# Optimization experiments

Hardware: AMD Instinct MI355X
Metric: run time of the kernel (lower is better)

The kernel has to match this reference:

```python
import jax, jax.numpy as jnp
import numpy as np

B = 8192; L = 68; NPG = L + 1; N = B * NPG
IN = 4; HID = 64; OUT = 7; NL = 8
BN_EPS = 1e-5


def setup_inputs() -> dict:
    key = jax.random.key(0)
    ks = jax.random.split(key, 12)
    # graph topology (same for every graph): ring among L landmarks + master node (idx L)
    # connected to every landmark; directed edges both ways (PyG-style edge_index).
    ring = np.stack([np.arange(L), (np.arange(L) + 1) % L])            # [2, L]
    mast = np.stack([np.arange(L), np.full(L, L)])                     # [2, L]
    und = np.concatenate([ring, mast], axis=1)                         # [2, 2L]
    e = np.concatenate([und, und[::-1]], axis=1)                       # [2, 4L]
    offs = (np.arange(B) * NPG)[:, None, None]
    edge_index = (e[None] + offs).transpose(1, 0, 2).reshape(2, -1)    # [2, B*4L]
    s = 1.0 / np.sqrt(HID)
    return {
        "x": jax.random.normal(ks[0], (N, IN), jnp.float32),
        "edge_index": jnp.asarray(edge_index, jnp.int32),
        "batch": jnp.repeat(jnp.arange(B, dtype=jnp.int32), NPG),
        "master_mask": jnp.tile(jnp.arange(NPG) == L, B),
        "conv_first_W": jax.random.normal(ks[1], (IN, HID), jnp.float32) * 0.5,
        "conv_first_b": jnp.zeros((HID,), jnp.float32),
        "conv_mid_W": jax.random.normal(ks[2], (NL - 2, HID, HID), jnp.float32) * s,
        "conv_mid_b": jnp.zeros((NL - 2, HID), jnp.float32),
        "conv_last_W": jax.random.normal(ks[3], (HID, HID), jnp.float32) * s,
        "conv_last_b": jnp.zeros((HID,), jnp.float32),
        "bn_gamma": jnp.ones((NL - 1, HID), jnp.float32),
        "bn_beta": jnp.zeros((NL - 1, HID), jnp.float32),
        "bn_mean": jax.random.normal(ks[4], (NL - 1, HID), jnp.float32) * 0.1,
        "bn_var": jax.random.uniform(ks[5], (NL - 1, HID), jnp.float32) * 0.5 + 0.5,
        "att_W1": jax.random.normal(ks[6], (HID, HID), jnp.float32) * s,
        "att_b1": jnp.zeros((HID,), jnp.float32),
        "att_W2": jax.random.normal(ks[7], (HID, 1), jnp.float32) * s,
        "att_b2": jnp.zeros((1,), jnp.float32),
        "fc1_W": jax.random.normal(ks[8], (3 * HID, HID), jnp.float32) / np.sqrt(3 * HID),
        "fc1_b": jnp.zeros((HID,), jnp.float32),
        "fc2_W": jax.random.normal(ks[9], (HID, OUT), jnp.float32) * s,
        "fc2_b": jnp.zeros((OUT,), jnp.float32),
    }


def reference(x, edge_index, batch, master_mask,
              conv_first_W, conv_first_b, conv_mid_W, conv_mid_b,
              conv_last_W, conv_last_b, bn_gamma, bn_beta, bn_mean, bn_var,
              att_W1, att_b1, att_W2, att_b2, fc1_W, fc1_b, fc2_W, fc2_b):
    n = x.shape[0]
    src, dst = edge_index[0], edge_index[1]
    # GCN symmetric normalization with self-loops: deg_i = 1 + in-degree
    deg = 1.0 + jax.ops.segment_sum(jnp.ones_like(src, x.dtype), dst, num_segments=n)
    dis = jax.lax.rsqrt(deg)
    enorm = (dis[src] * dis[dst])[:, None]                 # [E,1]
    self_norm = (1.0 / deg)[:, None]                       # [N,1] self-loop coeff

    def gcn(h, W, b):
        h = h @ W                                          # [N,HID]
        agg = jax.ops.segment_sum(h[src] * enorm, dst, num_segments=n)
        return agg + h * self_norm + b

    def bn(h, i):  # eval-mode BatchNorm1d
        return bn_gamma[i] * (h - bn_mean[i]) * jax.lax.rsqrt(bn_var[i] + BN_EPS) + bn_beta[i]

    h = bn(jax.nn.relu(gcn(x, conv_first_W, conv_first_b)), 0)
    for i in range(NL - 2):  # residual GCN blocks
        h = bn(jax.nn.relu(gcn(h, conv_mid_W[i], conv_mid_b[i])), i + 1) + h
    h = jax.nn.relu(gcn(h, conv_last_W, conv_last_b))

    mfl = master_mask.astype(h.dtype)                      # [N]
    mcnt = jax.ops.segment_sum(mfl, batch, num_segments=B)
    master = jax.ops.segment_sum(h * mfl[:, None], batch, num_segments=B) / mcnt[:, None]
    att = jax.nn.sigmoid(jax.nn.relu(master @ att_W1 + att_b1) @ att_W2 + att_b2)
    master = master * att

    rfl = 1.0 - mfl
    rcnt = jax.ops.segment_sum(rfl, batch, num_segments=B)
    x_mean = jax.ops.segment_sum(h * rfl[:, None], batch, num_segments=B) / rcnt[:, None]
    h_masked = jnp.where(master_mask[:, None], -jnp.inf, h)
    x_max = jax.ops.segment_max(h_masked, batch, num_segments=B)

    g = jnp.concatenate([x_mean, x_max, master], axis=1)   # [B, 3*HID]
    return jax.nn.relu(g @ fc1_W + fc1_b) @ fc2_W + fc2_b  # [B, OUT]
```

## Files before the change

kernel.cpp:

```cpp
#include <hip/hip_runtime.h>

typedef float f32x4 __attribute__((ext_vector_type(4)));
typedef short short8 __attribute__((ext_vector_type(8)));
typedef unsigned int u32;
typedef unsigned short u16;

#define CLL 0.25f
#define CML 0.06019292654288460f
#define SELFM 0.014492753623188406f

__device__ __forceinline__ u16 f2bf(float x) {
  u32 b = __float_as_uint(x);
  return (u16)((b + 0x7FFFu + ((b >> 16) & 1u)) >> 16);
}

__device__ __forceinline__ u32 cvtpk(float a, float b) {
  u32 r;
  asm("v_cvt_pk_bf16_f32 %0, %1, %2" : "=v"(r) : "v"(a), "v"(b));
  return r;
}

__global__ void prep(const float* __restrict__ midW, const float* __restrict__ lastW,
                     const float* __restrict__ bng, const float* __restrict__ bnb,
                     const float* __restrict__ bnm, const float* __restrict__ bnv,
                     u16* __restrict__ frag, float* __restrict__ bns) {
  const int t0 = blockIdx.x * blockDim.x + threadIdx.x;
  for (int u = t0; u < 7 * 4 * 2 * 64; u += gridDim.x * blockDim.x) {
    const int lane = u & 63;
    const int t = u >> 6;
    const int ks = t & 1;
    const int nt = (t >> 1) & 3;
    const int l = t >> 3;
    const float* W = (l < 6) ? (midW + l * 4096) : lastW;
    const int col = nt * 16 + (lane & 15);
    const int kb = ks * 32 + (lane >> 4) * 8;
    u16* dst = frag + (size_t)u * 8;
#pragma unroll
    for (int j = 0; j < 8; ++j) dst[j] = f2bf(W[(kb + j) * 64 + col]);
  }
  for (int u = t0; u < 7 * 64; u += gridDim.x * blockDim.x) {
    const int l = u >> 6, f = u & 63;
    const float sc = (float)((double)bng[l * 64 + f] / sqrt((double)bnv[l * 64 + f] + 1e-5));
    bns[l * 128 + f] = sc;
    bns[l * 128 + 64 + f] = bnb[l * 64 + f] - bnm[l * 64 + f] * sc;
  }
}

#define SUM4(V) ((V)[0] + (V)[1] + (V)[2] + (V)[3])
#define MAX4(V) fmaxf(fmaxf((V)[0], (V)[1]), fmaxf((V)[2], (V)[3]))

#define WADDR(MT, R) ((16 * (MT) + 4 * qg + (R)) * 64 + (cq ^ ((R) << 3)))

#define STEP(MT, T, TPM1, TNP1, H, RESID)                              \
  {                                                                    \
    const float sp = (qg == 3) ? TPM1[3] : T[3];                       \
    const float pv = __shfl(sp, (lane + 48) & 63, 64);                 \
    const float sn = (qg == 0) ? TNP1[0] : T[0];                       \
    const float nv = __shfl(sn, (lane + 16) & 63, 64);                 \
    const float ta0 = ((MT) == 0 && qg == 0) ? t4[3] : pv;             \
    const float tb3 = ((MT) == 4 && qg == 0) ? t0[0] : nv;             \
    float o0 = fmaf(CLL, ta0 + T[0] + T[1], cmt);                      \
    float o1 = fmaf(CLL, T[0] + T[1] + T[2], cmt);                     \
    float o2 = fmaf(CLL, T[1] + T[2] + T[3], cmt);                     \
    float o3 = fmaf(CLL, T[2] + T[3] + tb3, cmt);                      \
    o0 = fmaf(fmaxf(o0, 0.f), sc, sh);                                 \
    o1 = fmaf(fmaxf(o1, 0.f), sc, sh);                                 \
    o2 = fmaf(fmaxf(o2, 0.f), sc, sh);                                 \
    o3 = fmaf(fmaxf(o3, 0.f), sc, sh);                                 \
    if (RESID) { o0 += H[0]; o1 += H[1]; o2 += H[2]; o3 += H[3]; }     \
    H[0] = o0; H[1] = o1; H[2] = o2; H[3] = o3;                        \
  }

#define WPAIR(HW, MT, H)                                               \
  {                                                                    \
    const u32 pa = cvtpk(H[0], H[1]);                                  \
    const u32 pb = cvtpk(H[2], H[3]);                                  \
    (HW)[WADDR(MT, 0)] = (u16)pa;                                      \
    (HW)[WADDR(MT, 1)] = (u16)(pa >> 16);                              \
    (HW)[WADDR(MT, 2)] = (u16)pb;                                      \
    (HW)[WADDR(MT, 3)] = (u16)(pb >> 16);                              \
  }

#define EPILOG(RESID, WRITE, HBW)                                      \
  {                                                                    \
    float S = SUM4(t0) + SUM4(t1) + SUM4(t2) + SUM4(t3) + SUM4(t4);    \
    if (qg == 1) S -= t4[0];     \
    S += __shfl_xor(S, 16, 64);                                        \
    S += __shfl_xor(S, 32, 64);                                        \
    const float t68b = __shfl(t4[0], 16 + p15, 64);                    \
    const float cmt = fmaf(CML, t68b, bias);                           \
    float mv = fmaxf(fmaf(CML, S, fmaf(SELFM, t68b, bias)), 0.f);      \
    mv = fmaf(mv, sc, sh);                                             \
    if (RESID) mv += h4[0];                                            \
    STEP(0, t0, t4, t1, h0, RESID)                                     \
    STEP(1, t1, t0, t2, h1, RESID)                                     \
    STEP(2, t2, t1, t3, h2, RESID)                                     \
    STEP(3, t3, t2, t4, h3, RESID)                                     \
    STEP(4, t4, t3, t0, h4, RESID)                                     \
    if (qg == 1) h4[0] = mv;        \
    if (WRITE) {                                                       \
      u16* hw_ = (HBW);                                                \
      WPAIR(hw_, 0, h0)                                                \
      WPAIR(hw_, 1, h1)                                                \
      WPAIR(hw_, 2, h2)                                                \
      WPAIR(hw_, 3, h3)                                                \
      if (qg == 0) { WPAIR(hw_, 4, h4) }                               \
      else if (qg == 1) hw_[68 * 64 + (c ^ 32)] = (u16)cvtpk(h4[0], h4[0]); \
    }                                                                  \
  }

#define MP(HR, MT, T)                                                  \
  {                                                                    \
    const short8 a0 = *(const short8*)&(HR)[(MT) * 1024 + ra0];        \
    const short8 a1 = *(const short8*)&(HR)[(MT) * 1024 + ra1];        \
    f32x4 acc = {0.f, 0.f, 0.f, 0.f};                                  \
    acc = __builtin_amdgcn_mfma_f32_16x16x32_bf16(a0, b0, acc, 0, 0, 0); \
    acc = __builtin_amdgcn_mfma_f32_16x16x32_bf16(a1, b1, acc, 0, 0, 0); \
    T = acc;                                                           \
  }

__launch_bounds__(256)
__global__ void gcn_fused(
    const float* __restrict__ x,
    const float* __restrict__ cfW, const float* __restrict__ cfb,
    const float* __restrict__ cmb, const float* __restrict__ clb,
    const float* __restrict__ aW1, const float* __restrict__ ab1,
    const float* __restrict__ aW2, const float* __restrict__ ab2,
    const float* __restrict__ f1W, const float* __restrict__ f1b,
    const float* __restrict__ f2W, const float* __restrict__ f2b,
    const u16* __restrict__ frag, const float* __restrict__ bns,
    float* __restrict__ out) {
  __shared__ u16 hb[2][80 * 64];
  __shared__ float xl4[80 * 4];
  __shared__ float mrow[64];
  __shared__ float gv[192];
  __shared__ float part[256];

  const int tid = threadIdx.x;
  const int g = blockIdx.x;
  const int lane = tid & 63;
  const int wv = tid >> 6;
  const int p15 = lane & 15;
  const int qg = lane >> 4;
  const int c = wv * 16 + p15;
  const int cq = c ^ ((qg & 1) << 5);
  const int rsw = (p15 & 7) << 3;
  const int ra0 = (p15 * 64 + qg * 8) ^ rsw;
  const int ra1 = (p15 * 64 + 32 + qg * 8) ^ rsw;

  for (int i = tid; i < 5120; i += 256) ((u32*)hb)[i] = 0u;
  if (tid < 69)
    *(f32x4*)&xl4[tid * 4] = *(const f32x4*)&x[((size_t)g * 69 + tid) * 4];
  else if (tid < 80)
    *(f32x4*)&xl4[tid * 4] = (f32x4){0.f, 0.f, 0.f, 0.f};

  const u16* fb = frag + ((size_t)(0 * 4 + wv) * 2 * 64 + lane) * 8;
  short8 b0 = *(const short8*)fb;
  short8 b1 = *(const short8*)(fb + 512);

  f32x4 t0, t1, t2, t3, t4;
  f32x4 h0, h1, h2, h3, h4;

  __syncthreads();

  {
    const float w0 = cfW[c], w1 = cfW[64 + c], w2 = cfW[128 + c], w3 = cfW[192 + c];
#define L0T(MT, T)                                                     \
    { _Pragma("unroll") for (int r = 0; r < 4; ++r) {                  \
        const f32x4 xv = *(const f32x4*)&xl4[(16 * (MT) + 4 * qg + r) * 4]; \
        T[r] = fmaf(xv[0], w0, fmaf(xv[1], w1, fmaf(xv[2], w2, xv[3] * w3))); } }
    L0T(0, t0) L0T(1, t1) L0T(2, t2) L0T(3, t3) L0T(4, t4)
#undef L0T
  }
  {
    const float bias = cfb[c];
    const float sc = bns[c], sh = bns[64 + c];
    EPILOG(false, true, &hb[0][0])
  }
  __syncthreads();

  for (int l = 1; l <= 6; ++l) {
    const u16* fbn = frag + ((size_t)(l * 4 + wv) * 2 * 64 + lane) * 8;
    const short8 nb0 = *(const short8*)fbn;
    const short8 nb1 = *(const short8*)(fbn + 512);
    const u16* hr = &hb[(l + 1) & 1][0];
    MP(hr, 0, t0) MP(hr, 1, t1) MP(hr, 2, t2) MP(hr, 3, t3) MP(hr, 4, t4)
    b0 = nb0;
    b1 = nb1;
    const float bias = cmb[(l - 1) * 64 + c];
    const float sc = bns[l * 128 + c], sh = bns[l * 128 + 64 + c];
    EPILOG(true, true, &hb[l & 1][0])
    __syncthreads();
  }

  {
    const u16* hr = &hb[0][0];
    MP(hr, 0, t0) MP(hr, 1, t1) MP(hr, 2, t2) MP(hr, 3, t3) MP(hr, 4, t4)
    const float bias = clb[c];
    const float sc = 1.f, sh = 0.f;
    EPILOG(false, false, (u16*)nullptr)
  }

  {
    float s = SUM4(h0) + SUM4(h1) + SUM4(h2) + SUM4(h3);
    float mx = fmaxf(fmaxf(MAX4(h0), MAX4(h1)), fmaxf(MAX4(h2), MAX4(h3)));
    if (qg == 0) {
      s += SUM4(h4);
      mx = fmaxf(mx, MAX4(h4));
    }
    s += __shfl_xor(s, 16, 64);
    s += __shfl_xor(s, 32, 64);
    mx = fmaxf(mx, __shfl_xor(mx, 16, 64));
    mx = fmaxf(mx, __shfl_xor(mx, 32, 64));
    if (qg == 0) {
      gv[c] = s * (1.f / 68.f);
      gv[64 + c] = mx;
    }
    if (qg == 1) mrow[c] = h4[0];
  }
  __syncthreads();

  {
    float z = 0.f;
#pragma unroll
    for (int k = 0; k < 16; ++k)
      z = fmaf(mrow[wv * 16 + k], aW1[(wv * 16 + k) * 64 + lane], z);
    part[wv * 64 + lane] = z;
  }
  __syncthreads();
  if (tid < 64) {
    float z = part[tid] + part[64 + tid] + part[128 + tid] + part[192 + tid] + ab1[tid];
    z = fmaxf(z, 0.f);
    float pr = z * aW2[tid];
#pragma unroll
    for (int off = 32; off > 0; off >>= 1) pr += __shfl_xor(pr, off, 64);
    const float att = 1.f / (1.f + expf(-(pr + ab2[0])));
    gv[128 + tid] = mrow[tid] * att;
  }
  __syncthreads();

  {
    float a = 0.f;
#pragma unroll
    for (int i = 0; i < 48; ++i)
      a = fmaf(gv[wv * 48 + i], f1W[(wv * 48 + i) * 64 + lane], a);
    part[wv * 64 + lane] = a;
  }
  __syncthreads();
  if (tid < 64) {
    float a = part[tid] + part[64 + tid] + part[128 + tid] + part[192 + tid] + f1b[tid];
    const float y = fmaxf(a, 0.f);
    float po[7];
#pragma unroll
    for (int o = 0; o < 7; ++o) po[o] = y * f2W[tid * 7 + o];
#pragma unroll
    for (int o = 0; o < 7; ++o)
#pragma unroll
      for (int off = 32; off > 0; off >>= 1) po[o] += __shfl_xor(po[o], off, 64);
    if (tid == 0) {
#pragma unroll
      for (int o = 0; o < 7; ++o) out[(size_t)g * 7 + o] = po[o] + f2b[o];
    }
  }
}

extern "C" void kernel_launch(void* const* d_in, const int* in_sizes, int n_in,
                              void* d_out, int out_size, void* d_ws, size_t ws_size,
                              hipStream_t stream) {
  (void)in_sizes; (void)n_in; (void)ws_size;
  const float* x   = (const float*)d_in[0];
  const float* cfW = (const float*)d_in[4];
  const float* cfb = (const float*)d_in[5];
  const float* cmW = (const float*)d_in[6];
  const float* cmb = (const float*)d_in[7];
  const float* clW = (const float*)d_in[8];
  const float* clb = (const float*)d_in[9];
  const float* bng = (const float*)d_in[10];
  const float* bnb = (const float*)d_in[11];
  const float* bnm = (const float*)d_in[12];
  const float* bnv = (const float*)d_in[13];
  const float* aW1 = (const float*)d_in[14];
  const float* ab1 = (const float*)d_in[15];
  const float* aW2 = (const float*)d_in[16];
  const float* ab2 = (const float*)d_in[17];
  const float* f1W = (const float*)d_in[18];
  const float* f1b = (const float*)d_in[19];
  const float* f2W = (const float*)d_in[20];
  const float* f2b = (const float*)d_in[21];

  u16* frag = (u16*)d_ws;
  float* bns = (float*)((char*)d_ws + 57344);
  const int ngraphs = out_size / 7;

  prep<<<dim3(16), dim3(256), 0, stream>>>(cmW, clW, bng, bnb, bnm, bnv, frag, bns);
  gcn_fused<<<dim3(ngraphs), dim3(256), 0, stream>>>(
      x, cfW, cfb, cmb, clb, aW1, ab1, aW2, ab2, f1W, f1b, f2W, f2b,
      frag, bns, (float*)d_out);
}
```

Baseline: 154.7 us.

## Compute graph aggregation as MFMA with a constant normalized-adjacency matrix

Replaces the shuffle-based ring/master neighbor aggregation with a bf16 MFMA product between a precomputed 80x96 normalized adjacency fragment set and the transformed features, which are staged through a new swizzled LDS buffer. The prep kernel builds the adjacency fragments once, and each layer runs extra MFMAs plus LDS writes and reads. The aim is to replace many cross-lane shuffles and scalar adds with matrix-core work. In exchange it adds LDS traffic, roughly 12 more short8 registers, and bf16 rounding of the aggregated features.

```diff
diff --git a/kernel.cpp b/kernel.cpp
--- a/kernel.cpp
+++ b/kernel.cpp
@@ -4,6 +4,7 @@
 typedef short short8 __attribute__((ext_vector_type(8)));
 typedef unsigned int u32;
 typedef unsigned short u16;
+typedef u32 u32x2 __attribute__((ext_vector_type(2)));
 
 #define CLL 0.25f
 #define CML 0.06019292654288460f
@@ -13,7 +14,6 @@
   u32 b = __float_as_uint(x);
   return (u16)((b + 0x7FFFu + ((b >> 16) & 1u)) >> 16);
 }
-
 __device__ __forceinline__ u32 cvtpk(float a, float b) {
   u32 r;
   asm("v_cvt_pk_bf16_f32 %0, %1, %2" : "=v"(r) : "v"(a), "v"(b));
@@ -23,9 +23,11 @@
 __global__ void prep(const float* __restrict__ midW, const float* __restrict__ lastW,
                      const float* __restrict__ bng, const float* __restrict__ bnb,
                      const float* __restrict__ bnm, const float* __restrict__ bnv,
-                     u16* __restrict__ frag, float* __restrict__ bns) {
+                     u16* __restrict__ frag, float* __restrict__ bns,
+                     u16* __restrict__ afr) {
   const int t0 = blockIdx.x * blockDim.x + threadIdx.x;
-  for (int u = t0; u < 7 * 4 * 2 * 64; u += gridDim.x * blockDim.x) {
+  const int stride = gridDim.x * blockDim.x;
+  for (int u = t0; u < 7 * 4 * 2 * 64; u += stride) {
     const int lane = u & 63;
     const int t = u >> 6;
     const int ks = t & 1;
@@ -38,85 +40,101 @@
 #pragma unroll
     for (int j = 0; j < 8; ++j) dst[j] = f2bf(W[(kb + j) * 64 + col]);
   }
-  for (int u = t0; u < 7 * 64; u += gridDim.x * blockDim.x) {
+  for (int u = t0; u < 7 * 64; u += stride) {
     const int l = u >> 6, f = u & 63;
     const float sc = (float)((double)bng[l * 64 + f] / sqrt((double)bnv[l * 64 + f] + 1e-5));
     bns[l * 128 + f] = sc;
     bns[l * 128 + 64 + f] = bnb[l * 64 + f] - bnm[l * 64 + f] * sc;
   }
+  const int MTs[12] = {0, 1, 2, 4, 1, 2, 3, 4, 0, 1, 3, 4};
+  const int KSs[12] = {0, 0, 0, 0, 1, 1, 1, 1, 2, 2, 2, 2};
+  for (int u = t0; u < 12 * 64; u += stride) {
+    const int p = u >> 6, lane = u & 63;
+    const int r = MTs[p] * 16 + (lane & 15);
+    const int kb = KSs[p] * 32 + ((lane >> 4) << 3);
+    u16* dst = afr + (size_t)u * 8;
+#pragma unroll
+    for (int j = 0; j < 8; ++j) {
+      const int k = kb + j;
+      float v = 0.f;
+      if (r < 68) {
+        if (k < 68) {
+          if (k == r || k == (r + 1) % 68 || k == (r + 67) % 68) v = CLL;
+        } else if (k == 68) {
+          v = CML;
+        }
+      } else if (r == 68) {
+        if (k < 68) v = CML;
+        else if (k == 68) v = SELFM;
+      }
+      dst[j] = f2bf(v);
+    }
+  }
 }
 
 #define SUM4(V) ((V)[0] + (V)[1] + (V)[2] + (V)[3])
 #define MAX4(V) fmaxf(fmaxf((V)[0], (V)[1]), fmaxf((V)[2], (V)[3]))
-
-#define WADDR(MT, R) ((16 * (MT) + 4 * qg + (R)) * 64 + (cq ^ ((R) << 3)))
-
-#define STEP(MT, T, TPM1, TNP1, H, RESID)                              \
-  {                                                                    \
-    const float sp = (qg == 3) ? TPM1[3] : T[3];                       \
-    const float pv = __shfl(sp, (lane + 48) & 63, 64);                 \
-    const float sn = (qg == 0) ? TNP1[0] : T[0];                       \
-    const float nv = __shfl(sn, (lane + 16) & 63, 64);                 \
-    const float ta0 = ((MT) == 0 && qg == 0) ? t4[3] : pv;             \
-    const float tb3 = ((MT) == 4 && qg == 0) ? t0[0] : nv;             \
-    float o0 = fmaf(CLL, ta0 + T[0] + T[1], cmt);                      \
-    float o1 = fmaf(CLL, T[0] + T[1] + T[2], cmt);                     \
-    float o2 = fmaf(CLL, T[1] + T[2] + T[3], cmt);                     \
-    float o3 = fmaf(CLL, T[2] + T[3] + tb3, cmt);                      \
-    o0 = fmaf(fmaxf(o0, 0.f), sc, sh);                                 \
-    o1 = fmaf(fmaxf(o1, 0.f), sc, sh);                                 \
-    o2 = fmaf(fmaxf(o2, 0.f), sc, sh);                                 \
-    o3 = fmaf(fmaxf(o3, 0.f), sc, sh);                                 \
-    if (RESID) { o0 += H[0]; o1 += H[1]; o2 += H[2]; o3 += H[3]; }     \
-    H[0] = o0; H[1] = o1; H[2] = o2; H[3] = o3;                        \
-  }
-
-#define WPAIR(HW, MT, H)                                               \
-  {                                                                    \
-    const u32 pa = cvtpk(H[0], H[1]);                                  \
-    const u32 pb = cvtpk(H[2], H[3]);                                  \
-    (HW)[WADDR(MT, 0)] = (u16)pa;                                      \
-    (HW)[WADDR(MT, 1)] = (u16)(pa >> 16);                              \
-    (HW)[WADDR(MT, 2)] = (u16)pb;                                      \
-    (HW)[WADDR(MT, 3)] = (u16)(pb >> 16);                              \
-  }
-
-#define EPILOG(RESID, WRITE, HBW)                                      \
-  {                                                                    \
-    float S = SUM4(t0) + SUM4(t1) + SUM4(t2) + SUM4(t3) + SUM4(t4);    \
-    if (qg == 1) S -= t4[0];     \
-    S += __shfl_xor(S, 16, 64);                                        \
-    S += __shfl_xor(S, 32, 64);                                        \
-    const float t68b = __shfl(t4[0], 16 + p15, 64);                    \
-    const float cmt = fmaf(CML, t68b, bias);                           \
-    float mv = fmaxf(fmaf(CML, S, fmaf(SELFM, t68b, bias)), 0.f);      \
-    mv = fmaf(mv, sc, sh);                                             \
-    if (RESID) mv += h4[0];                                            \
-    STEP(0, t0, t4, t1, h0, RESID)                                     \
-    STEP(1, t1, t0, t2, h1, RESID)                                     \
-    STEP(2, t2, t1, t3, h2, RESID)                                     \
-    STEP(3, t3, t2, t4, h3, RESID)                                     \
-    STEP(4, t4, t3, t0, h4, RESID)                                     \
-    if (qg == 1) h4[0] = mv;        \
-    if (WRITE) {                                                       \
-      u16* hw_ = (HBW);                                                \
-      WPAIR(hw_, 0, h0)                                                \
-      WPAIR(hw_, 1, h1)                                                \
-      WPAIR(hw_, 2, h2)                                                \
-      WPAIR(hw_, 3, h3)                                                \
-      if (qg == 0) { WPAIR(hw_, 4, h4) }                               \
-      else if (qg == 1) hw_[68 * 64 + (c ^ 32)] = (u16)cvtpk(h4[0], h4[0]); \
-    }                                                                  \
-  }
-
-#define MP(HR, MT, T)                                                  \
-  {                                                                    \
-    const short8 a0 = *(const short8*)&(HR)[(MT) * 1024 + ra0];        \
-    const short8 a1 = *(const short8*)&(HR)[(MT) * 1024 + ra1];        \
-    f32x4 acc = {0.f, 0.f, 0.f, 0.f};                                  \
-    acc = __builtin_amdgcn_mfma_f32_16x16x32_bf16(a0, b0, acc, 0, 0, 0); \
-    acc = __builtin_amdgcn_mfma_f32_16x16x32_bf16(a1, b1, acc, 0, 0, 0); \
-    T = acc;                                                           \
+#define MM(A, B, C) __builtin_amdgcn_mfma_f32_16x16x32_bf16(A, B, C, 0, 0, 0)
+
+#define MP2(HR, MT, T)                                                   \
+  {                                                                      \
+    const short8 a0 = *(const short8*)&(HR)[(MT) * 1024 + ra0];          \
+    const short8 a1 = *(const short8*)&(HR)[(MT) * 1024 + ra1];          \
+    f32x4 acc = z4;                                                      \
+    acc = MM(a0, b0, acc);                                               \
+    acc = MM(a1, b1, acc);                                               \
+    T = acc;                                                             \
+  }
+
+#define UWR(OFF, U)                                                      \
+  {                                                                      \
+    u32x2 w;                                                             \
+    w.x = cvtpk(U[0], U[1]);                                             \
+    w.y = cvtpk(U[2], U[3]);                                             \
+    *(u32x2*)((char*)ucm + (OFF)) = w;                                   \
+  }
+
+#define EPI2BN(AG, H, RESID)                                             \
+  {                                                                      \
+    _Pragma("unroll") for (int e = 0; e < 4; ++e) {                      \
+      float v = fmaxf(AG[e] + bias, 0.f);                                \
+      v = fmaf(v, sc, sh);                                               \
+      if (RESID) v += H[e];                                              \
+      H[e] = v;                                                          \
+    }                                                                    \
+  }
+
+#define WPAIR(HW, MT, H)                                                 \
+  {                                                                      \
+    const u32 pa = cvtpk(H[0], H[1]);                                    \
+    const u32 pb = cvtpk(H[2], H[3]);                                    \
+    (HW)[(MT) * 1024 + 0 * 64 + wr0] = (u16)pa;                          \
+    (HW)[(MT) * 1024 + 1 * 64 + wr1] = (u16)(pa >> 16);                  \
+    (HW)[(MT) * 1024 + 2 * 64 + wr2] = (u16)pb;                          \
+    (HW)[(MT) * 1024 + 3 * 64 + wr3] = (u16)(pb >> 16);                  \
+  }
+
+#define AGG_EPI(HW, RESID, WRITE_H)                                      \
+  {                                                                      \
+    const short8 ub0 = *(const short8*)((const char*)ucm + urb);         \
+    const short8 ub1 = *(const short8*)((const char*)ucm + urb + 64);    \
+    const short8 ub2 = *(const short8*)((const char*)ucm + urb + 128);   \
+    f32x4 ag;                                                            \
+    ag = MM(F8, ub2, MM(F0, ub0, z4));                                   \
+    EPI2BN(ag, h0, RESID);                                               \
+    if (WRITE_H) WPAIR(HW, 0, h0);                                       \
+    ag = MM(F9, ub2, MM(F4, ub1, MM(F1, ub0, z4)));                      \
+    EPI2BN(ag, h1, RESID);                                               \
+    if (WRITE_H) WPAIR(HW, 1, h1);                                       \
+    ag = MM(F9, ub2, MM(F5, ub1, MM(F2, ub0, z4)));                      \
+    EPI2BN(ag, h2, RESID);                                               \
+    if (WRITE_H) WPAIR(HW, 2, h2);                                       \
+    ag = MM(F10, ub2, MM(F6, ub1, z4));                                  \
+    EPI2BN(ag, h3, RESID);                                               \
+    if (WRITE_H) WPAIR(HW, 3, h3);                                       \
+    ag = MM(F11, ub2, MM(F7, ub1, MM(F3, ub0, z4)));                     \
+    EPI2BN(ag, h4, RESID);                                               \
+    if (WRITE_H) WPAIR(HW, 4, h4);                                       \
   }
 
 __launch_bounds__(256)
@@ -129,8 +147,10 @@
     const float* __restrict__ f1W, const float* __restrict__ f1b,
     const float* __restrict__ f2W, const float* __restrict__ f2b,
     const u16* __restrict__ frag, const float* __restrict__ bns,
+    const u16* __restrict__ afr,
     float* __restrict__ out) {
   __shared__ u16 hb[2][80 * 64];
+  __shared__ __align__(16) u16 ucm[64 * 96];
   __shared__ float xl4[80 * 4];
   __shared__ float mrow[64];
   __shared__ float gv[192];
@@ -143,62 +163,103 @@
   const int p15 = lane & 15;
   const int qg = lane >> 4;
   const int c = wv * 16 + p15;
-  const int cq = c ^ ((qg & 1) << 5);
+  const f32x4 z4 = {0.f, 0.f, 0.f, 0.f};
+
   const int rsw = (p15 & 7) << 3;
   const int ra0 = (p15 * 64 + qg * 8) ^ rsw;
   const int ra1 = (p15 * 64 + 32 + qg * 8) ^ rsw;
-
-  for (int i = tid; i < 5120; i += 256) ((u32*)hb)[i] = 0u;
+  const int cq = c ^ ((qg & 1) << 5);
+  const int wr0 = qg * 256 + cq;
+  const int wr1 = qg * 256 + (cq ^ 8);
+  const int wr2 = qg * 256 + (cq ^ 16);
+  const int wr3 = qg * 256 + (cq ^ 24);
+  const int e3 = c & 3;
+  const int q1 = qg >> 1;
+  const int q0 = (qg & 1) << 3;
+  const int cb = c * 192;
+  const int uw0 = cb + (((0 + q1) ^ e3) << 4) + q0;
+  const int uw1 = cb + (((2 + q1) ^ e3) << 4) + q0;
+  const int uw2 = cb + (((4 + q1) ^ e3) << 4) + q0;
+  const int uw3 = cb + (((6 + q1) ^ e3) << 4) + q0;
+  const int uw4 = cb + (((8 + q1) ^ e3) << 4) + q0;
+  const int urb = cb + ((qg ^ e3) << 4);
+
+  const u16* ap = afr + (size_t)lane * 8;
+  const short8 F0 = *(const short8*)(ap);
+  const short8 F1 = *(const short8*)(ap + 512);
+  const short8 F2 = *(const short8*)(ap + 1024);
+  const short8 F3 = *(const short8*)(ap + 1536);
+  const short8 F4 = *(const short8*)(ap + 2048);
+  const short8 F5 = *(const short8*)(ap + 2560);
+  const short8 F6 = *(const short8*)(ap + 3072);
+  const short8 F7 = *(const short8*)(ap + 3584);
+  const short8 F8 = *(const short8*)(ap + 4096);
+  const short8 F9 = *(const short8*)(ap + 4608);
+  const short8 F10 = *(const short8*)(ap + 5120);
+  const short8 F11 = *(const short8*)(ap + 5632);
+
+  const u16* fb1 = frag + ((size_t)(0 * 4 + wv) * 2 * 64 + lane) * 8;
+  short8 b0 = *(const short8*)fb1;
+  short8 b1 = *(const short8*)(fb1 + 512);
+
+  {
+    f32x4* ucz = (f32x4*)ucm;
+#pragma unroll
+    for (int it = 0; it < 3; ++it) ucz[tid + it * 256] = z4;
+  }
   if (tid < 69)
     *(f32x4*)&xl4[tid * 4] = *(const f32x4*)&x[((size_t)g * 69 + tid) * 4];
   else if (tid < 80)
-    *(f32x4*)&xl4[tid * 4] = (f32x4){0.f, 0.f, 0.f, 0.f};
-
-  const u16* fb = frag + ((size_t)(0 * 4 + wv) * 2 * 64 + lane) * 8;
-  short8 b0 = *(const short8*)fb;
-  short8 b1 = *(const short8*)(fb + 512);
-
-  f32x4 t0, t1, t2, t3, t4;
+    *(f32x4*)&xl4[tid * 4] = z4;
+
   f32x4 h0, h1, h2, h3, h4;
 
   __syncthreads();
 
   {
     const float w0 = cfW[c], w1 = cfW[64 + c], w2 = cfW[128 + c], w3 = cfW[192 + c];
-#define L0T(MT, T)                                                     \
-    { _Pragma("unroll") for (int r = 0; r < 4; ++r) {                  \
+    f32x4 u0, u1, u2, u3, u4;
+#define L0T(MT, T)                                                          \
+    { _Pragma("unroll") for (int r = 0; r < 4; ++r) {                       \
         const f32x4 xv = *(const f32x4*)&xl4[(16 * (MT) + 4 * qg + r) * 4]; \
         T[r] = fmaf(xv[0], w0, fmaf(xv[1], w1, fmaf(xv[2], w2, xv[3] * w3))); } }
-    L0T(0, t0) L0T(1, t1) L0T(2, t2) L0T(3, t3) L0T(4, t4)
+    L0T(0, u0) L0T(1, u1) L0T(2, u2) L0T(3, u3) L0T(4, u4)
 #undef L0T
-  }
-  {
+    UWR(uw0, u0) UWR(uw1, u1) UWR(uw2, u2) UWR(uw3, u3) UWR(uw4, u4)
     const float bias = cfb[c];
     const float sc = bns[c], sh = bns[64 + c];
-    EPILOG(false, true, &hb[0][0])
-  }
-  __syncthreads();
-
+    u16* hw = &hb[0][0];
+    AGG_EPI(hw, false, true)
+  }
+  __syncthreads();
+
+#pragma unroll 1
   for (int l = 1; l <= 6; ++l) {
     const u16* fbn = frag + ((size_t)(l * 4 + wv) * 2 * 64 + lane) * 8;
     const short8 nb0 = *(const short8*)fbn;
     const short8 nb1 = *(const short8*)(fbn + 512);
+    const float bias = cmb[(l - 1) * 64 + c];
+    const float sc = bns[l * 128 + c];
+    const float sh = bns[l * 128 + 64 + c];
     const u16* hr = &hb[(l + 1) & 1][0];
-    MP(hr, 0, t0) MP(hr, 1, t1) MP(hr, 2, t2) MP(hr, 3, t3) MP(hr, 4, t4)
+    u16* hw = &hb[l & 1][0];
+    f32x4 u0, u1, u2, u3, u4;
+    MP2(hr, 0, u0) MP2(hr, 1, u1) MP2(hr, 2, u2) MP2(hr, 3, u3) MP2(hr, 4, u4)
+    UWR(uw0, u0) UWR(uw1, u1) UWR(uw2, u2) UWR(uw3, u3) UWR(uw4, u4)
     b0 = nb0;
     b1 = nb1;
-    const float bias = cmb[(l - 1) * 64 + c];
-    const float sc = bns[l * 128 + c], sh = bns[l * 128 + 64 + c];
-    EPILOG(true, true, &hb[l & 1][0])
+    AGG_EPI(hw, true, true)
     __syncthreads();
   }
 
   {
     const u16* hr = &hb[0][0];
-    MP(hr, 0, t0) MP(hr, 1, t1) MP(hr, 2, t2) MP(hr, 3, t3) MP(hr, 4, t4)
+    f32x4 u0, u1, u2, u3, u4;
+    MP2(hr, 0, u0) MP2(hr, 1, u1) MP2(hr, 2, u2) MP2(hr, 3, u3) MP2(hr, 4, u4)
+    UWR(uw0, u0) UWR(uw1, u1) UWR(uw2, u2) UWR(uw3, u3) UWR(uw4, u4)
     const float bias = clb[c];
     const float sc = 1.f, sh = 0.f;
-    EPILOG(false, false, (u16*)nullptr)
+    AGG_EPI((u16*)nullptr, false, false)
   }
 
   {
@@ -288,12 +349,13 @@
   const float* f2W = (const float*)d_in[20];
   const float* f2b = (const float*)d_in[21];
 
-  u16* frag = (u16*)d_ws;
+  u16* frag  = (u16*)d_ws;
   float* bns = (float*)((char*)d_ws + 57344);
+  u16* afr   = (u16*)((char*)d_ws + 57344 + 3584);
   const int ngraphs = out_size / 7;
 
-  prep<<<dim3(16), dim3(256), 0, stream>>>(cmW, clW, bng, bnb, bnm, bnv, frag, bns);
+  prep<<<dim3(16), dim3(256), 0, stream>>>(cmW, clW, bng, bnb, bnm, bnv, frag, bns, afr);
   gcn_fused<<<dim3(ngraphs), dim3(256), 0, stream>>>(
       x, cfW, cfb, cmb, clb, aW1, ab1, aW2, ab2, f1W, f1b, f2W, f2b,
-      frag, bns, (float*)d_out);
-}
+      frag, bns, afr, (float*)d_out);
+}
```

New measurement: 163.5 us. 1.06x slower.

## Halve block to two waves each computing two column tiles per graph

Applied to the files above, without the earlier changes.

Each graph's block shrinks from four waves to two, and every wave now computes two 16-column output tiles. The A fragments read from LDS are reused across both tiles, and the neighbour shuffles pack the two tiles' values into one bf16 pair so a single shuffle serves both. LDS zeroing is cut to only the padding rows. The aim is less LDS traffic, fewer shuffles and more resident blocks, in exchange for higher register pressure per wave and bf16 rounding of the shuffled neighbour values.

```diff
diff --git a/kernel.cpp b/kernel.cpp
--- a/kernel.cpp
+++ b/kernel.cpp
@@ -13,7 +13,6 @@
   u32 b = __float_as_uint(x);
   return (u16)((b + 0x7FFFu + ((b >> 16) & 1u)) >> 16);
 }
-
 __device__ __forceinline__ u32 cvtpk(float a, float b) {
   u32 r;
   asm("v_cvt_pk_bf16_f32 %0, %1, %2" : "=v"(r) : "v"(a), "v"(b));
@@ -49,77 +48,108 @@
 #define SUM4(V) ((V)[0] + (V)[1] + (V)[2] + (V)[3])
 #define MAX4(V) fmaxf(fmaxf((V)[0], (V)[1]), fmaxf((V)[2], (V)[3]))
 
-#define WADDR(MT, R) ((16 * (MT) + 4 * qg + (R)) * 64 + (cq ^ ((R) << 3)))
-
-#define STEP(MT, T, TPM1, TNP1, H, RESID)                              \
+#define STEP2(MT, TA, TPA, TNA, TB, TPB, TNB, HA, HB, RESID)           \
   {                                                                    \
-    const float sp = (qg == 3) ? TPM1[3] : T[3];                       \
-    const float pv = __shfl(sp, (lane + 48) & 63, 64);                 \
-    const float sn = (qg == 0) ? TNP1[0] : T[0];                       \
-    const float nv = __shfl(sn, (lane + 16) & 63, 64);                 \
-    const float ta0 = ((MT) == 0 && qg == 0) ? t4[3] : pv;             \
-    const float tb3 = ((MT) == 4 && qg == 0) ? t0[0] : nv;             \
-    float o0 = fmaf(CLL, ta0 + T[0] + T[1], cmt);                      \
-    float o1 = fmaf(CLL, T[0] + T[1] + T[2], cmt);                     \
-    float o2 = fmaf(CLL, T[1] + T[2] + T[3], cmt);                     \
-    float o3 = fmaf(CLL, T[2] + T[3] + tb3, cmt);                      \
-    o0 = fmaf(fmaxf(o0, 0.f), sc, sh);                                 \
-    o1 = fmaf(fmaxf(o1, 0.f), sc, sh);                                 \
-    o2 = fmaf(fmaxf(o2, 0.f), sc, sh);                                 \
-    o3 = fmaf(fmaxf(o3, 0.f), sc, sh);                                 \
-    if (RESID) { o0 += H[0]; o1 += H[1]; o2 += H[2]; o3 += H[3]; }     \
-    H[0] = o0; H[1] = o1; H[2] = o2; H[3] = o3;                        \
-  }
-
-#define WPAIR(HW, MT, H)                                               \
+    const float spA_ = (qg == 3) ? TPA[3] : TA[3];                     \
+    const float spB_ = (qg == 3) ? TPB[3] : TB[3];                     \
+    const u32 pvP_ = (u32)__shfl((int)cvtpk(spA_, spB_), (lane + 48) & 63, 64); \
+    const float snA_ = (qg == 0) ? TNA[0] : TA[0];                     \
+    const float snB_ = (qg == 0) ? TNB[0] : TB[0];                     \
+    const u32 nvP_ = (u32)__shfl((int)cvtpk(snA_, snB_), (lane + 16) & 63, 64); \
+    const float pvA_ = __uint_as_float(pvP_ << 16);                    \
+    const float pvB_ = __uint_as_float(pvP_ & 0xffff0000u);            \
+    const float nvA_ = __uint_as_float(nvP_ << 16);                    \
+    const float nvB_ = __uint_as_float(nvP_ & 0xffff0000u);            \
+    const float ta0A_ = ((MT) == 0 && qg == 0) ? tA4[3] : pvA_;        \
+    const float ta0B_ = ((MT) == 0 && qg == 0) ? tB4[3] : pvB_;        \
+    const float tb3A_ = ((MT) == 4 && qg == 0) ? tA0[0] : nvA_;        \
+    const float tb3B_ = ((MT) == 4 && qg == 0) ? tB0[0] : nvB_;        \
+    float oA0 = fmaf(CLL, ta0A_ + TA[0] + TA[1], cmtA_);               \
+    float oA1 = fmaf(CLL, TA[0] + TA[1] + TA[2], cmtA_);               \
+    float oA2 = fmaf(CLL, TA[1] + TA[2] + TA[3], cmtA_);               \
+    float oA3 = fmaf(CLL, TA[2] + TA[3] + tb3A_, cmtA_);               \
+    float oB0 = fmaf(CLL, ta0B_ + TB[0] + TB[1], cmtB_);               \
+    float oB1 = fmaf(CLL, TB[0] + TB[1] + TB[2], cmtB_);               \
+    float oB2 = fmaf(CLL, TB[1] + TB[2] + TB[3], cmtB_);               \
+    float oB3 = fmaf(CLL, TB[2] + TB[3] + tb3B_, cmtB_);               \
+    oA0 = fmaf(fmaxf(oA0, 0.f), scA_, shA_);                           \
+    oA1 = fmaf(fmaxf(oA1, 0.f), scA_, shA_);                           \
+    oA2 = fmaf(fmaxf(oA2, 0.f), scA_, shA_);                           \
+    oA3 = fmaf(fmaxf(oA3, 0.f), scA_, shA_);                           \
+    oB0 = fmaf(fmaxf(oB0, 0.f), scB_, shB_);                           \
+    oB1 = fmaf(fmaxf(oB1, 0.f), scB_, shB_);                           \
+    oB2 = fmaf(fmaxf(oB2, 0.f), scB_, shB_);                           \
+    oB3 = fmaf(fmaxf(oB3, 0.f), scB_, shB_);                           \
+    if (RESID) {                                                       \
+      oA0 += HA[0]; oA1 += HA[1]; oA2 += HA[2]; oA3 += HA[3];          \
+      oB0 += HB[0]; oB1 += HB[1]; oB2 += HB[2]; oB3 += HB[3];          \
+    }                                                                  \
+    HA[0] = oA0; HA[1] = oA1; HA[2] = oA2; HA[3] = oA3;                \
+    HB[0] = oB0; HB[1] = oB1; HB[2] = oB2; HB[3] = oB3;                \
+  }
+
+#define WPAIR2(HW, MT, H, CQ)                                          \
   {                                                                    \
     const u32 pa = cvtpk(H[0], H[1]);                                  \
     const u32 pb = cvtpk(H[2], H[3]);                                  \
-    (HW)[WADDR(MT, 0)] = (u16)pa;                                      \
-    (HW)[WADDR(MT, 1)] = (u16)(pa >> 16);                              \
-    (HW)[WADDR(MT, 2)] = (u16)pb;                                      \
-    (HW)[WADDR(MT, 3)] = (u16)(pb >> 16);                              \
-  }
-
-#define EPILOG(RESID, WRITE, HBW)                                      \
+    (HW)[(16 * (MT) + 4 * qg + 0) * 64 + (CQ)] = (u16)pa;              \
+    (HW)[(16 * (MT) + 4 * qg + 1) * 64 + ((CQ) ^ 8)] = (u16)(pa >> 16);\
+    (HW)[(16 * (MT) + 4 * qg + 2) * 64 + ((CQ) ^ 16)] = (u16)pb;       \
+    (HW)[(16 * (MT) + 4 * qg + 3) * 64 + ((CQ) ^ 24)] = (u16)(pb >> 16); \
+  }
+
+#define EPILOG2(RESID, WRITE, HBW, BA, BB, SCA, SHA, SCB, SHB)         \
   {                                                                    \
-    float S = SUM4(t0) + SUM4(t1) + SUM4(t2) + SUM4(t3) + SUM4(t4);    \
-    if (qg == 1) S -= t4[0];     \
-    S += __shfl_xor(S, 16, 64);                                        \
-    S += __shfl_xor(S, 32, 64);                                        \
-    const float t68b = __shfl(t4[0], 16 + p15, 64);                    \
-    const float cmt = fmaf(CML, t68b, bias);                           \
-    float mv = fmaxf(fmaf(CML, S, fmaf(SELFM, t68b, bias)), 0.f);      \
-    mv = fmaf(mv, sc, sh);                                             \
-    if (RESID) mv += h4[0];                                            \
-    STEP(0, t0, t4, t1, h0, RESID)                                     \
-    STEP(1, t1, t0, t2, h1, RESID)                                     \
-    STEP(2, t2, t1, t3, h2, RESID)                                     \
-    STEP(3, t3, t2, t4, h3, RESID)                                     \
-    STEP(4, t4, t3, t0, h4, RESID)                                     \
-    if (qg == 1) h4[0] = mv;        \
+    float SA_ = SUM4(tA0) + SUM4(tA1) + SUM4(tA2) + SUM4(tA3) + SUM4(tA4); \
+    float SB_ = SUM4(tB0) + SUM4(tB1) + SUM4(tB2) + SUM4(tB3) + SUM4(tB4); \
+    if (qg == 1) { SA_ -= tA4[0]; SB_ -= tB4[0]; }                     \
+    SA_ += __shfl_xor(SA_, 16, 64);                                    \
+    SA_ += __shfl_xor(SA_, 32, 64);                                    \
+    SB_ += __shfl_xor(SB_, 16, 64);                                    \
+    SB_ += __shfl_xor(SB_, 32, 64);                                    \
+    const u32 pk_ = (u32)__shfl((int)cvtpk(tA4[0], tB4[0]), 16 + p15, 64); \
+    const float scA_ = (SCA), shA_ = (SHA), scB_ = (SCB), shB_ = (SHB);\
+    const float cmtA_ = fmaf(CML, __uint_as_float(pk_ << 16), (BA));   \
+    const float cmtB_ = fmaf(CML, __uint_as_float(pk_ & 0xffff0000u), (BB)); \
+    float mvA_ = 0.f, mvB_ = 0.f;                                      \
+    if (qg == 1) {                                                     \
+      mvA_ = fmaf(fmaxf(fmaf(CML, SA_, fmaf(SELFM, tA4[0], (BA))), 0.f), scA_, shA_); \
+      mvB_ = fmaf(fmaxf(fmaf(CML, SB_, fmaf(SELFM, tB4[0], (BB))), 0.f), scB_, shB_); \
+      if (RESID) { mvA_ += hA4[0]; mvB_ += hB4[0]; }                   \
+    }                                                                  \
+    STEP2(0, tA0, tA4, tA1, tB0, tB4, tB1, hA0, hB0, RESID)            \
+    STEP2(1, tA1, tA0, tA2, tB1, tB0, tB2, hA1, hB1, RESID)            \
+    STEP2(2, tA2, tA1, tA3, tB2, tB1, tB3, hA2, hB2, RESID)            \
+    STEP2(3, tA3, tA2, tA4, tB3, tB2, tB4, hA3, hB3, RESID)            \
+    STEP2(4, tA4, tA3, tA0, tB4, tB3, tB0, hA4, hB4, RESID)            \
+    if (qg == 1) { hA4[0] = mvA_; hB4[0] = mvB_; }                     \
     if (WRITE) {                                                       \
       u16* hw_ = (HBW);                                                \
-      WPAIR(hw_, 0, h0)                                                \
-      WPAIR(hw_, 1, h1)                                                \
-      WPAIR(hw_, 2, h2)                                                \
-      WPAIR(hw_, 3, h3)                                                \
-      if (qg == 0) { WPAIR(hw_, 4, h4) }                               \
-      else if (qg == 1) hw_[68 * 64 + (c ^ 32)] = (u16)cvtpk(h4[0], h4[0]); \
+      WPAIR2(hw_, 0, hA0, cqA) WPAIR2(hw_, 0, hB0, cqB)                \
+      WPAIR2(hw_, 1, hA1, cqA) WPAIR2(hw_, 1, hB1, cqB)                \
+      WPAIR2(hw_, 2, hA2, cqA) WPAIR2(hw_, 2, hB2, cqB)                \
+      WPAIR2(hw_, 3, hA3, cqA) WPAIR2(hw_, 3, hB3, cqB)                \
+      if (qg == 0) { WPAIR2(hw_, 4, hA4, cqA) WPAIR2(hw_, 4, hB4, cqB) } \
+      else if (qg == 1) {                                              \
+        hw_[68 * 64 + (cA ^ 32)] = (u16)cvtpk(mvA_, mvA_);             \
+        hw_[68 * 64 + (cB ^ 32)] = (u16)cvtpk(mvB_, mvB_);             \
+      }                                                                \
     }                                                                  \
   }
 
-#define MP(HR, MT, T)                                                  \
+#define MM(A, B, C) __builtin_amdgcn_mfma_f32_16x16x32_bf16(A, B, C, 0, 0, 0)
+
+#define MP3(HR, MT, TA, TB)                                            \
   {                                                                    \
     const short8 a0 = *(const short8*)&(HR)[(MT) * 1024 + ra0];        \
     const short8 a1 = *(const short8*)&(HR)[(MT) * 1024 + ra1];        \
-    f32x4 acc = {0.f, 0.f, 0.f, 0.f};                                  \
-    acc = __builtin_amdgcn_mfma_f32_16x16x32_bf16(a0, b0, acc, 0, 0, 0); \
-    acc = __builtin_amdgcn_mfma_f32_16x16x32_bf16(a1, b1, acc, 0, 0, 0); \
-    T = acc;                                                           \
-  }
-
-__launch_bounds__(256)
+    f32x4 accA = z4, accB = z4;                                        \
+    accA = MM(a0, bA0, accA); accA = MM(a1, bA1, accA);                \
+    accB = MM(a0, bB0, accB); accB = MM(a1, bB1, accB);                \
+    TA = accA; TB = accB;                                              \
+  }
+
+__launch_bounds__(128)
 __global__ void gcn_fused(
     const float* __restrict__ x,
     const float* __restrict__ cfW, const float* __restrict__ cfb,
@@ -134,102 +164,129 @@
   __shared__ float xl4[80 * 4];
   __shared__ float mrow[64];
   __shared__ float gv[192];
-  __shared__ float part[256];
+  __shared__ float part[128];
 
   const int tid = threadIdx.x;
   const int g = blockIdx.x;
   const int lane = tid & 63;
-  const int wv = tid >> 6;
+  const int w = tid >> 6;
   const int p15 = lane & 15;
   const int qg = lane >> 4;
-  const int c = wv * 16 + p15;
-  const int cq = c ^ ((qg & 1) << 5);
+  const int cA = w * 32 + p15;
+  const int cB = cA + 16;
+  const f32x4 z4 = {0.f, 0.f, 0.f, 0.f};
+
   const int rsw = (p15 & 7) << 3;
   const int ra0 = (p15 * 64 + qg * 8) ^ rsw;
   const int ra1 = (p15 * 64 + 32 + qg * 8) ^ rsw;
-
-  for (int i = tid; i < 5120; i += 256) ((u32*)hb)[i] = 0u;
+  const int cqA = cA ^ ((qg & 1) << 5);
+  const int cqB = cqA ^ 16;
+
+  const u16* f0p = frag + (((size_t)(2 * w) * 2) * 64 + lane) * 8;
+  const u16* f1p = frag + (((size_t)(2 * w + 1) * 2) * 64 + lane) * 8;
+  short8 bA0 = *(const short8*)f0p;
+  short8 bA1 = *(const short8*)(f0p + 512);
+  short8 bB0 = *(const short8*)f1p;
+  short8 bB1 = *(const short8*)(f1p + 512);
+
+  {
+    u32* hz = (u32*)hb;
+#pragma unroll
+    for (int it = 0; it < 3; ++it) {
+      const int i = tid + it * 128;
+      if (i < 352) {
+        hz[2208 + i] = 0u;
+        hz[2560 + 2208 + i] = 0u;
+      }
+    }
+  }
   if (tid < 69)
     *(f32x4*)&xl4[tid * 4] = *(const f32x4*)&x[((size_t)g * 69 + tid) * 4];
   else if (tid < 80)
-    *(f32x4*)&xl4[tid * 4] = (f32x4){0.f, 0.f, 0.f, 0.f};
-
-  const u16* fb = frag + ((size_t)(0 * 4 + wv) * 2 * 64 + lane) * 8;
-  short8 b0 = *(const short8*)fb;
-  short8 b1 = *(const short8*)(fb + 512);
-
-  f32x4 t0, t1, t2, t3, t4;
-  f32x4 h0, h1, h2, h3, h4;
-
-  __syncthreads();
-
-  {
-    const float w0 = cfW[c], w1 = cfW[64 + c], w2 = cfW[128 + c], w3 = cfW[192 + c];
-#define L0T(MT, T)                                                     \
+    *(f32x4*)&xl4[tid * 4] = z4;
+
+  f32x4 tA0, tA1, tA2, tA3, tA4, tB0, tB1, tB2, tB3, tB4;
+  f32x4 hA0, hA1, hA2, hA3, hA4, hB0, hB1, hB2, hB3, hB4;
+
+  __syncthreads();
+
+  {
+    const float wA0 = cfW[cA], wA1 = cfW[64 + cA], wA2 = cfW[128 + cA], wA3 = cfW[192 + cA];
+    const float wB0 = cfW[cB], wB1 = cfW[64 + cB], wB2 = cfW[128 + cB], wB3 = cfW[192 + cB];
+#define L0T(MT, TA, TB)                                                \
     { _Pragma("unroll") for (int r = 0; r < 4; ++r) {                  \
         const f32x4 xv = *(const f32x4*)&xl4[(16 * (MT) + 4 * qg + r) * 4]; \
-        T[r] = fmaf(xv[0], w0, fmaf(xv[1], w1, fmaf(xv[2], w2, xv[3] * w3))); } }
-    L0T(0, t0) L0T(1, t1) L0T(2, t2) L0T(3, t3) L0T(4, t4)
+        TA[r] = fmaf(xv[0], wA0, fmaf(xv[1], wA1, fmaf(xv[2], wA2, xv[3] * wA3))); \
+        TB[r] = fmaf(xv[0], wB0, fmaf(xv[1], wB1, fmaf(xv[2], wB2, xv[3] * wB3))); } }
+    L0T(0, tA0, tB0) L0T(1, tA1, tB1) L0T(2, tA2, tB2) L0T(3, tA3, tB3) L0T(4, tA4, tB4)
 #undef L0T
   }
-  {
-    const float bias = cfb[c];
-    const float sc = bns[c], sh = bns[64 + c];
-    EPILOG(false, true, &hb[0][0])
-  }
-  __syncthreads();
-
+  EPILOG2(false, true, &hb[0][0], cfb[cA], cfb[cB], bns[cA], bns[64 + cA],
+          bns[cB], bns[64 + cB])
+  __syncthreads();
+
+#pragma unroll 1
   for (int l = 1; l <= 6; ++l) {
-    const u16* fbn = frag + ((size_t)(l * 4 + wv) * 2 * 64 + lane) * 8;
-    const short8 nb0 = *(const short8*)fbn;
-    const short8 nb1 = *(const short8*)(fbn + 512);
+    const u16* fA = frag + ((((size_t)l * 4 + 2 * w) * 2) * 64 + lane) * 8;
+    const u16* fB = frag + ((((size_t)l * 4 + 2 * w + 1) * 2) * 64 + lane) * 8;
+    const short8 nA0 = *(const short8*)fA;
+    const short8 nA1 = *(const short8*)(fA + 512);
+    const short8 nB0 = *(const short8*)fB;
+    const short8 nB1 = *(const short8*)(fB + 512);
+    const float biasA = cmb[(l - 1) * 64 + cA];
+    const float biasB = cmb[(l - 1) * 64 + cB];
+    const float lscA = bns[l * 128 + cA], lshA = bns[l * 128 + 64 + cA];
+    const float lscB = bns[l * 128 + cB], lshB = bns[l * 128 + 64 + cB];
     const u16* hr = &hb[(l + 1) & 1][0];
-    MP(hr, 0, t0) MP(hr, 1, t1) MP(hr, 2, t2) MP(hr, 3, t3) MP(hr, 4, t4)
-    b0 = nb0;
-    b1 = nb1;
-    const float bias = cmb[(l - 1) * 64 + c];
-    const float sc = bns[l * 128 + c], sh = bns[l * 128 + 64 + c];
-    EPILOG(true, true, &hb[l & 1][0])
+    MP3(hr, 0, tA0, tB0) MP3(hr, 1, tA1, tB1) MP3(hr, 2, tA2, tB2)
+    MP3(hr, 3, tA3, tB3) MP3(hr, 4, tA4, tB4)
+    bA0 = nA0; bA1 = nA1; bB0 = nB0; bB1 = nB1;
+    EPILOG2(true, true, &hb[l & 1][0], biasA, biasB, lscA, lshA, lscB, lshB)
     __syncthreads();
   }
 
   {
     const u16* hr = &hb[0][0];
-    MP(hr, 0, t0) MP(hr, 1, t1) MP(hr, 2, t2) MP(hr, 3, t3) MP(hr, 4, t4)
-    const float bias = clb[c];
-    const float sc = 1.f, sh = 0.f;
-    EPILOG(false, false, (u16*)nullptr)
-  }
-
-  {
-    float s = SUM4(h0) + SUM4(h1) + SUM4(h2) + SUM4(h3);
-    float mx = fmaxf(fmaxf(MAX4(h0), MAX4(h1)), fmaxf(MAX4(h2), MAX4(h3)));
+    MP3(hr, 0, tA0, tB0) MP3(hr, 1, tA1, tB1) MP3(hr, 2, tA2, tB2)
+    MP3(hr, 3, tA3, tB3) MP3(hr, 4, tA4, tB4)
+    EPILOG2(false, false, (u16*)nullptr, clb[cA], clb[cB], 1.f, 0.f, 1.f, 0.f)
+  }
+
+  {
+    float sA = SUM4(hA0) + SUM4(hA1) + SUM4(hA2) + SUM4(hA3);
+    float sB = SUM4(hB0) + SUM4(hB1) + SUM4(hB2) + SUM4(hB3);
+    float mA = fmaxf(fmaxf(MAX4(hA0), MAX4(hA1)), fmaxf(MAX4(hA2), MAX4(hA3)));
+    float mB = fmaxf(fmaxf(MAX4(hB0), MAX4(hB1)), fmaxf(MAX4(hB2), MAX4(hB3)));
     if (qg == 0) {
-      s += SUM4(h4);
-      mx = fmaxf(mx, MAX4(h4));
+      sA += SUM4(hA4); mA = fmaxf(mA, MAX4(hA4));
+      sB += SUM4(hB4); mB = fmaxf(mB, MAX4(hB4));
     }
-    s += __shfl_xor(s, 16, 64);
-    s += __shfl_xor(s, 32, 64);
-    mx = fmaxf(mx, __shfl_xor(mx, 16, 64));
-    mx = fmaxf(mx, __shfl_xor(mx, 32, 64));
+    sA += __shfl_xor(sA, 16, 64); sA += __shfl_xor(sA, 32, 64);
+    sB += __shfl_xor(sB, 16, 64); sB += __shfl_xor(sB, 32, 64);
+    mA = fmaxf(mA, __shfl_xor(mA, 16, 64)); mA = fmaxf(mA, __shfl_xor(mA, 32, 64));
+    mB = fmaxf(mB, __shfl_xor(mB, 16, 64)); mB = fmaxf(mB, __shfl_xor(mB, 32, 64));
     if (qg == 0) {
-      gv[c] = s * (1.f / 68.f);
-      gv[64 + c] = mx;
+      gv[cA] = sA * (1.f / 68.f);
+      gv[64 + cA] = mA;
+      gv[cB] = sB * (1.f / 68.f);
+      gv[64 + cB] = mB;
     }
-    if (qg == 1) mrow[c] = h4[0];
-  }
-  __syncthreads();
-
-  {
+    if (qg == 1) { mrow[cA] = hA4[0]; mrow[cB] = hB4[0]; }
+  }
+  __syncthreads();
+
+  {
+    const int f = tid & 63;
+    const int kh = tid >> 6;
     float z = 0.f;
 #pragma unroll
-    for (int k = 0; k < 16; ++k)
-      z = fmaf(mrow[wv * 16 + k], aW1[(wv * 16 + k) * 64 + lane], z);
-    part[wv * 64 + lane] = z;
+    for (int k = 0; k < 32; ++k)
+      z = fmaf(mrow[kh * 32 + k], aW1[(kh * 32 + k) * 64 + f], z);
+    part[tid] = z;
   }
   __syncthreads();
   if (tid < 64) {
-    float z = part[tid] + part[64 + tid] + part[128 + tid] + part[192 + tid] + ab1[tid];
+    float z = part[tid] + part[64 + tid] + ab1[tid];
     z = fmaxf(z, 0.f);
     float pr = z * aW2[tid];
 #pragma unroll
@@ -240,15 +297,17 @@
   __syncthreads();
 
   {
+    const int f = tid & 63;
+    const int ih = tid >> 6;
     float a = 0.f;
 #pragma unroll
-    for (int i = 0; i < 48; ++i)
-      a = fmaf(gv[wv * 48 + i], f1W[(wv * 48 + i) * 64 + lane], a);
-    part[wv * 64 + lane] = a;
+    for (int i = 0; i < 96; ++i)
+      a = fmaf(gv[ih * 96 + i], f1W[(ih * 96 + i) * 64 + f], a);
+    part[tid] = a;
   }
   __syncthreads();
   if (tid < 64) {
-    float a = part[tid] + part[64 + tid] + part[128 + tid] + part[192 + tid] + f1b[tid];
+    float a = part[tid] + part[64 + tid] + f1b[tid];
     const float y = fmaxf(a, 0.f);
     float po[7];
 #pragma unroll
@@ -293,7 +352,7 @@
   const int ngraphs = out_size / 7;
 
   prep<<<dim3(16), dim3(256), 0, stream>>>(cmW, clW, bng, bnb, bnm, bnv, frag, bns);
-  gcn_fused<<<dim3(ngraphs), dim3(256), 0, stream>>>(
+  gcn_fused<<<dim3(ngraphs), dim3(128), 0, stream>>>(
       x, cfW, cfb, cmb, clb, aW1, ab1, aW2, ab2, f1W, f1b, f2W, f2b,
       frag, bns, (float*)d_out);
 }
```

Result: no change. 157.0 us (+1.5%).
